# Optimization experiments

Measured on AMD Instinct MI355X. Metric: run time of the kernel, lower is better.

The kernel has to match this reference:

```python
import jax, jax.numpy as jnp
import numpy as np


def setup_inputs() -> dict:
    key = jax.random.key(0)
    kq, kk, kv = jax.random.split(key, 3)
    B, S, D = 4, 4096, 64
    Q = jax.random.normal(kq, (B, S, D), dtype=jnp.float32)
    K = jax.random.normal(kk, (B, S, D), dtype=jnp.float32)
    V = jax.random.normal(kv, (B, S, D), dtype=jnp.float32)
    return {"Q": Q, "K": K, "V": V}


def reference(Q, K, V):
    # nom = Q @ K^T  -> [B, Sq, Sk]
    # Original code does K.transpose_(1,2) in place BEFORE reading K.shape[1],
    # so demon = sqrt(d_head) (standard scaling).
    d = K.shape[-1]
    scores = jnp.einsum('bqd,bkd->bqk', Q, K) / jnp.sqrt(jnp.float32(d))
    # Faithful quirk: nn.Softmax(dim=1) normalizes over the QUERY axis (axis=1).
    attn = jax.nn.softmax(scores, axis=1)
    return jnp.einsum('bqk,bkd->bqd', attn, V)
```

## Files before the change

### kernel.cpp

```cpp
#include <hip/hip_runtime.h>


#define B_N 4
#define S_N 4096
#define D_N 64
#define BS_N (B_N * S_N)
#define NCHUNK 128
#define IMG_CH 8192
#define IMG_CH16 4096
#define QSC (0.125f * 1.44269504088896f)

typedef __attribute__((ext_vector_type(4))) float f32x4;
typedef __attribute__((ext_vector_type(2))) float f32x2;
typedef __attribute__((ext_vector_type(8))) short short8;
typedef __attribute__((ext_vector_type(8))) _Float16 half8;
typedef unsigned char uchar;

#define MFMA16(A, Bf, C) __builtin_amdgcn_mfma_f32_16x16x32_bf16((A), (Bf), (C), 0, 0, 0)
#define MFMAH(A, Bf, C) __builtin_amdgcn_mfma_f32_16x16x32_f16((A), (Bf), (C), 0, 0, 0)

__device__ __forceinline__ void split1(float x, unsigned short& h, unsigned short& l) {
  union { float f; unsigned u; } t; t.f = x;
  h = (unsigned short)(t.u >> 16);
  union { unsigned u; float f; } hv; hv.u = ((unsigned)h) << 16;
  union { float f; unsigned u; } r; r.f = x - hv.f;
  l = (unsigned short)(r.u >> 16);
}

__device__ __forceinline__ void splitFrag8(const f32x4 a, const f32x4 b, short8& hi, short8& lo) {
#pragma unroll
  for (int j = 0; j < 4; ++j) { unsigned short h, l; split1(a[j], h, l); hi[j] = (short)h; lo[j] = (short)l; }
#pragma unroll
  for (int j = 0; j < 4; ++j) { unsigned short h, l; split1(b[j], h, l); hi[4 + j] = (short)h; lo[4 + j] = (short)l; }
}

__device__ __forceinline__ void gld16(const void* g, void* l) {
  __builtin_amdgcn_global_load_lds((const __attribute__((address_space(1))) unsigned int*)g,
                                   (__attribute__((address_space(3))) unsigned int*)l, 16, 0, 0);
}

__global__ __launch_bounds__(256) void sdpa_prepKQ(const float* __restrict__ K,
                                                   const float* __restrict__ Qm,
                                                   uchar* __restrict__ Khl,
                                                   uchar* __restrict__ K16,
                                                   uchar* __restrict__ Q16) {
  const int sel = blockIdx.x >> 9;
  const int c = blockIdx.x & 127;
  const int b = (blockIdx.x >> 7) & 3;
  const int t = threadIdx.x;
  const int r = t >> 3;
  const int d0 = (t & 7) * 8;
  const float* src = (sel ? Qm : K) + ((size_t)(b * S_N + c * 32 + r)) * D_N + d0;
  f32x4 x0 = *(const f32x4*)(src);
  f32x4 x1 = *(const f32x4*)(src + 4);
  const int kt = r >> 4;
  const int lane = ((d0 & 31) >> 3) * 16 + (r & 15);
  const size_t ch16 = ((size_t)(b * NCHUNK + c)) * IMG_CH16 + kt * 2048 + (d0 >> 5) * 1024 + lane * 16;

  if (sel == 0) {
    short8 h8, l8;
    splitFrag8(x0, x1, h8, l8);
    const int ph = d0 >> 5;
    uchar* base = Khl + ((size_t)(b * NCHUNK + c)) * IMG_CH + kt * 4096 + lane * 16;
    *(short8*)(base + ph * 1024) = h8;
    *(short8*)(base + (2 + ph) * 1024) = l8;
    half8 hf;
#pragma unroll
    for (int j = 0; j < 4; ++j) { hf[j] = (_Float16)x0[j]; hf[4 + j] = (_Float16)x1[j]; }
    *(half8*)(K16 + ch16) = hf;
  } else {
    x0 *= QSC; x1 *= QSC;
    half8 hf;
#pragma unroll
    for (int j = 0; j < 4; ++j) { hf[j] = (_Float16)x0[j]; hf[4 + j] = (_Float16)x1[j]; }
    *(half8*)(Q16 + ch16) = hf;
  }
}

__global__ __launch_bounds__(256, 4) void sdpa_stats16(const uchar* __restrict__ K16,
                                                       const uchar* __restrict__ Q16,
                                                       float* __restrict__ lPart) {
  const int tid = threadIdx.x, lane = tid & 63, w = tid >> 6;
  const int l15 = lane & 15, g4 = lane >> 4;
  const int xcd = blockIdx.x & 7;
  const int b = xcd >> 1;
  const int r = blockIdx.x >> 3;
  const int kt = ((r & 31) << 1) | (xcd & 1);
  const int qs = ((r >> 5) << 2) | w;

  half8 kf[4][2];
#pragma unroll
  for (int kg = 0; kg < 4; ++kg) {
    const uchar* kc = K16 + ((size_t)(b * NCHUNK + kt * 2 + (kg >> 1))) * IMG_CH16
                    + (kg & 1) * 2048 + lane * 16;
    kf[kg][0] = *(const half8*)(kc);
    kf[kg][1] = *(const half8*)(kc + 1024);
  }

  float lacc[4][4];
#pragma unroll
  for (int kg = 0; kg < 4; ++kg)
#pragma unroll
    for (int rr = 0; rr < 4; ++rr) lacc[kg][rr] = 0.f;

  const uchar* Qbase = Q16 + ((size_t)(b * NCHUNK + qs * 8)) * IMG_CH16 + lane * 16;

#pragma unroll 1
  for (int it = 0; it < 8; ++it) {
    const uchar* Qc = Qbase + (size_t)it * IMG_CH16;
#pragma unroll
    for (int qt = 0; qt < 2; ++qt) {
      half8 qf0 = *(const half8*)(Qc + qt * 2048);
      half8 qf1 = *(const half8*)(Qc + qt * 2048 + 1024);
#pragma unroll
      for (int kg = 0; kg < 4; ++kg) {
        f32x4 acc = {0.f, 0.f, 0.f, 0.f};
        acc = MFMAH(kf[kg][0], qf0, acc);
        acc = MFMAH(kf[kg][1], qf1, acc);
#pragma unroll
        for (int rr = 0; rr < 4; ++rr)
          lacc[kg][rr] += exp2f(acc[rr]);
      }
    }
  }

#pragma unroll
  for (int off = 1; off < 16; off <<= 1)
#pragma unroll
    for (int kg = 0; kg < 4; ++kg)
#pragma unroll
      for (int rr = 0; rr < 4; ++rr)
        lacc[kg][rr] += __shfl_xor(lacc[kg][rr], off);

  if (l15 == 0) {
#pragma unroll
    for (int kg = 0; kg < 4; ++kg)
#pragma unroll
      for (int rr = 0; rr < 4; ++rr)
        lPart[(size_t)qs * BS_N + b * S_N + kt * 64 + kg * 16 + (g4 << 2) + rr] = lacc[kg][rr];
  }
}

__global__ __launch_bounds__(256) void sdpa_prepV8(const float* __restrict__ V,
                                                   const float* __restrict__ lPart,
                                                   uchar* __restrict__ VT) {
  __shared__ float Vs[32][65];
  __shared__ float rls[32];
  const int c = blockIdx.x & 127;
  const int b = blockIdx.x >> 7;
  const int t = threadIdx.x;
  {
    const int k = t >> 3;
    const int d0 = (t & 7) * 8;
    const float* src = V + ((size_t)(b * S_N + c * 32 + k)) * D_N + d0;
    f32x4 x0 = *(const f32x4*)(src);
    f32x4 x1 = *(const f32x4*)(src + 4);
#pragma unroll
    for (int j = 0; j < 4; ++j) { Vs[k][d0 + j] = x0[j]; Vs[k][d0 + 4 + j] = x1[j]; }
    if (t < 32) {
      float s = 0.f;
      const float* lp = lPart + b * S_N + c * 32 + t;
#pragma unroll
      for (int j = 0; j < 16; ++j) s += lp[(size_t)j * BS_N];
      rls[t] = 1.0f / s;
    }
  }
  __syncthreads();
  const int d = t >> 2;
  const int kg = t & 3;
  half8 hf;
#pragma unroll
  for (int j = 0; j < 8; ++j) {
    const int cc = kg * 8 + j;
    const int k = (((cc >> 2) & 1) << 4) + (((cc >> 3)) << 2) + (cc & 3);
    hf[j] = (_Float16)(Vs[k][d] * rls[k]);
  }
  const int lane = kg * 16 + (d & 15);
  *(half8*)(VT + ((size_t)(b * NCHUNK + c)) * IMG_CH16 + (d >> 4) * 1024 + lane * 16) = hf;
}

__global__ __launch_bounds__(1024, 4) void sdpa_apply18(const float* __restrict__ Q,
                                                        const uchar* __restrict__ Kimg,
                                                        const uchar* __restrict__ VTimg,
                                                        float* __restrict__ Out) {
  __shared__ __attribute__((aligned(16))) uchar sm[69632];

  const int tid = threadIdx.x, lane = tid & 63, w = tid >> 6;
  const int l15 = lane & 15, g4 = lane >> 4;
  const int qsub = w >> 3, kq = w & 7;
  const int xcd = blockIdx.x & 7;
  const int b = xcd >> 1;
  const int qt = ((blockIdx.x >> 3) << 1) | (xcd & 1);

  short8 qh[2][2], ql[2][2];
#pragma unroll
  for (int qg = 0; qg < 2; ++qg) {
    const int qRow = qt * 64 + qsub * 32 + qg * 16 + l15;
    const float* Qp = Q + ((size_t)(b * S_N + qRow)) * D_N;
    f32x4 x0 = *(const f32x4*)(Qp + g4 * 8);
    f32x4 x1 = *(const f32x4*)(Qp + g4 * 8 + 4);
    f32x4 y0 = *(const f32x4*)(Qp + 32 + g4 * 8);
    f32x4 y1 = *(const f32x4*)(Qp + 36 + g4 * 8);
    x0 *= QSC; x1 *= QSC; y0 *= QSC; y1 *= QSC;
    splitFrag8(x0, x1, qh[qg][0], ql[qg][0]);
    splitFrag8(y0, y1, qh[qg][1], ql[qg][1]);
  }

  f32x4 accO[2][4];
#pragma unroll
  for (int qg = 0; qg < 2; ++qg)
#pragma unroll
    for (int dt = 0; dt < 4; ++dt) accO[qg][dt] = (f32x4){0.f, 0.f, 0.f, 0.f};

  const uchar* Kc = Kimg + ((size_t)(b * NCHUNK + kq * 16)) * IMG_CH + lane * 16;
  const uchar* Vc = VTimg + ((size_t)(b * NCHUNK + kq * 16)) * IMG_CH16 + lane * 16;
  uchar* const slab0 = sm + kq * 8192;
  const int l16 = lane * 16;

  half8 paF[2];

#define QK_FROM(KB)                                                            \
  _Pragma("unroll")                                                            \
  for (int kt = 0; kt < 2; ++kt) {                                             \
    short8 ah0 = KB[kt][0], ah1 = KB[kt][1];                                   \
    short8 al0 = KB[kt][2], al1 = KB[kt][3];                                   \
    _Pragma("unroll")                                                          \
    for (int qg = 0; qg < 2; ++qg) {                                           \
      f32x4 acc = {0.f, 0.f, 0.f, 0.f};                                        \
      acc = MFMA16(al0, qh[qg][0], acc);                                       \
      acc = MFMA16(ah0, ql[qg][0], acc);                                       \
      acc = MFMA16(ah0, qh[qg][0], acc);                                       \
      acc = MFMA16(al1, qh[qg][1], acc);                                       \
      acc = MFMA16(ah1, ql[qg][1], acc);                                       \
      acc = MFMA16(ah1, qh[qg][1], acc);                                       \
      _Pragma("unroll")                                                        \
      for (int rr = 0; rr < 4; ++rr)                                           \
        paF[qg][kt * 4 + rr] = (_Float16)exp2f(acc[rr]);                       \
    }                                                                          \
  }

#define PV_STEP(SLAB)                                                          \
  {                                                                            \
    _Pragma("unroll")                                                          \
    for (int dt = 0; dt < 4; ++dt) {                                           \
      half8 vf = *(const half8*)((SLAB) + dt * 1024 + l16);                    \
      _Pragma("unroll")                                                        \
      for (int qg = 0; qg < 2; ++qg)                                           \
        accO[qg][dt] = MFMAH(paF[qg], vf, accO[qg][dt]);                       \
    }                                                                          \
  }

  {
    short8 kb[2][4];
#pragma unroll
    for (int kt = 0; kt < 2; ++kt)
#pragma unroll
      for (int p = 0; p < 4; ++p)
        kb[kt][p] = *(const short8*)(Kc + (kt * 4 + p) * 1024);
    if (qsub == 0) {
#pragma unroll
      for (int s = 0; s < 4; ++s)
        gld16(Vc + s * 1024, slab0 + s * 1024);
    }
    QK_FROM(kb)
    asm volatile("s_waitcnt vmcnt(0)" ::: "memory");
    __syncthreads();
  }

#pragma unroll 1
  for (int it = 1; it < 16; ++it) {
    short8 kb[2][4];
    {
      const uchar* Kn = Kc + (size_t)it * IMG_CH;
#pragma unroll
      for (int kt = 0; kt < 2; ++kt)
#pragma unroll
        for (int p = 0; p < 4; ++p)
          kb[kt][p] = *(const short8*)(Kn + (kt * 4 + p) * 1024);
    }
    __builtin_amdgcn_sched_barrier(0);

    PV_STEP(slab0 + ((it - 1) & 1) * 4096)

    __builtin_amdgcn_sched_barrier(0);

    if (qsub == 0) {
      const uchar* Vn = Vc + (size_t)it * IMG_CH16;
      uchar* slabW = slab0 + (it & 1) * 4096;
#pragma unroll
      for (int s = 0; s < 4; ++s)
        gld16(Vn + s * 1024, slabW + s * 1024);
    }

    QK_FROM(kb)

    asm volatile("s_waitcnt vmcnt(0)" ::: "memory");
    __syncthreads();
  }

  PV_STEP(slab0 + 4096)

#undef QK_FROM
#undef PV_STEP

  float* Comb = (float*)sm;
#pragma unroll
  for (int qg = 0; qg < 2; ++qg) {
    __syncthreads();
    {
      float* CombW = Comb + w * (16 * 68);
#pragma unroll
      for (int dt = 0; dt < 4; ++dt)
#pragma unroll
        for (int r = 0; r < 4; ++r)
          CombW[((g4 << 2) + r) * 68 + dt * 16 + l15] = accO[qg][dt][r];
    }
    __syncthreads();
    {
      const int qs2 = tid >> 9;
      const int row = (tid >> 5) & 15;
      const int c2 = (tid & 31) * 2;
      f32x2 s = {0.f, 0.f};
#pragma unroll
      for (int kq2 = 0; kq2 < 8; ++kq2)
        s += *(const f32x2*)(Comb + (qs2 * 8 + kq2) * (16 * 68) + row * 68 + c2);
      *(f32x2*)(Out + ((size_t)(b * S_N + qt * 64 + qs2 * 32 + qg * 16 + row)) * D_N + c2) = s;
    }
  }
}

extern "C" void kernel_launch(void* const* d_in, const int* in_sizes, int n_in,
                              void* d_out, int out_size, void* d_ws, size_t ws_size,
                              hipStream_t stream) {
  (void)in_sizes; (void)n_in; (void)out_size;
  const float* Q = (const float*)d_in[0];
  const float* K = (const float*)d_in[1];
  const float* V = (const float*)d_in[2];
  float* out = (float*)d_out;
  uchar* ws = (uchar*)d_ws;

  const size_t offKhl = 0;
  const size_t offK16 = (size_t)B_N * NCHUNK * IMG_CH;
  const size_t offQ16 = offK16 + (size_t)B_N * NCHUNK * IMG_CH16;
  const size_t offLP = offQ16 + (size_t)B_N * NCHUNK * IMG_CH16;
  const size_t need = offLP + (size_t)16 * BS_N * 4;

  if (ws_size < need) return;
  float* lPart = (float*)(ws + offLP);

  sdpa_prepKQ<<<dim3(1024), dim3(256), 0, stream>>>(K, Q, ws + offKhl, ws + offK16, ws + offQ16);
  sdpa_stats16<<<dim3(1024), dim3(256), 0, stream>>>(ws + offK16, ws + offQ16, lPart);
  sdpa_prepV8<<<dim3(512), dim3(256), 0, stream>>>(V, lPart, ws + offQ16);
  sdpa_apply18<<<dim3(256), dim3(1024), 0, stream>>>(Q, ws + offKhl, ws + offQ16, out);
}
```

Baseline: 75.19 us.

## Use single fp16 QK products in apply kernel and stage K through LDS

The apply kernel no longer computes QK^T with a three-term bf16 hi/lo split. It now issues a single fp16 MFMA pair using the K16 image already produced for the stats pass, which removes the Khl image and its split work in the prep kernel. K is now staged into LDS with global_load_lds alongside V: one wave group loads K and the other loads V, into double-buffered slabs, with the shared buffer enlarged to 128KB. This cuts MFMA count and global traffic but lowers score precision to fp16, and the larger LDS footprint may limit occupancy.

```diff
diff --git a/kernel.cpp b/kernel.cpp
--- a/kernel.cpp
+++ b/kernel.cpp
@@ -6,44 +6,25 @@
 #define D_N 64
 #define BS_N (B_N * S_N)
 #define NCHUNK 128
-#define IMG_CH 8192
 #define IMG_CH16 4096
 #define QSC (0.125f * 1.44269504088896f)
 
 typedef __attribute__((ext_vector_type(4))) float f32x4;
 typedef __attribute__((ext_vector_type(2))) float f32x2;
-typedef __attribute__((ext_vector_type(8))) short short8;
 typedef __attribute__((ext_vector_type(8))) _Float16 half8;
 typedef unsigned char uchar;
 
-#define MFMA16(A, Bf, C) __builtin_amdgcn_mfma_f32_16x16x32_bf16((A), (Bf), (C), 0, 0, 0)
 #define MFMAH(A, Bf, C) __builtin_amdgcn_mfma_f32_16x16x32_f16((A), (Bf), (C), 0, 0, 0)
-
-__device__ __forceinline__ void split1(float x, unsigned short& h, unsigned short& l) {
-  union { float f; unsigned u; } t; t.f = x;
-  h = (unsigned short)(t.u >> 16);
-  union { unsigned u; float f; } hv; hv.u = ((unsigned)h) << 16;
-  union { float f; unsigned u; } r; r.f = x - hv.f;
-  l = (unsigned short)(r.u >> 16);
-}
-
-__device__ __forceinline__ void splitFrag8(const f32x4 a, const f32x4 b, short8& hi, short8& lo) {
-#pragma unroll
-  for (int j = 0; j < 4; ++j) { unsigned short h, l; split1(a[j], h, l); hi[j] = (short)h; lo[j] = (short)l; }
-#pragma unroll
-  for (int j = 0; j < 4; ++j) { unsigned short h, l; split1(b[j], h, l); hi[4 + j] = (short)h; lo[4 + j] = (short)l; }
-}
 
 __device__ __forceinline__ void gld16(const void* g, void* l) {
   __builtin_amdgcn_global_load_lds((const __attribute__((address_space(1))) unsigned int*)g,
                                    (__attribute__((address_space(3))) unsigned int*)l, 16, 0, 0);
 }
 
-__global__ __launch_bounds__(256) void sdpa_prepKQ(const float* __restrict__ K,
-                                                   const float* __restrict__ Qm,
-                                                   uchar* __restrict__ Khl,
-                                                   uchar* __restrict__ K16,
-                                                   uchar* __restrict__ Q16) {
+__global__ __launch_bounds__(256) void sdpa_prepKQ19(const float* __restrict__ K,
+                                                     const float* __restrict__ Qm,
+                                                     uchar* __restrict__ K16,
+                                                     uchar* __restrict__ Q16) {
   const int sel = blockIdx.x >> 9;
   const int c = blockIdx.x & 127;
   const int b = (blockIdx.x >> 7) & 3;
@@ -53,28 +34,15 @@
   const float* src = (sel ? Qm : K) + ((size_t)(b * S_N + c * 32 + r)) * D_N + d0;
   f32x4 x0 = *(const f32x4*)(src);
   f32x4 x1 = *(const f32x4*)(src + 4);
+  const float scale = sel ? QSC : 1.0f;
+  x0 *= scale; x1 *= scale;
+  half8 hf;
+#pragma unroll
+  for (int j = 0; j < 4; ++j) { hf[j] = (_Float16)x0[j]; hf[4 + j] = (_Float16)x1[j]; }
   const int kt = r >> 4;
   const int lane = ((d0 & 31) >> 3) * 16 + (r & 15);
-  const size_t ch16 = ((size_t)(b * NCHUNK + c)) * IMG_CH16 + kt * 2048 + (d0 >> 5) * 1024 + lane * 16;
-
-  if (sel == 0) {
-    short8 h8, l8;
-    splitFrag8(x0, x1, h8, l8);
-    const int ph = d0 >> 5;
-    uchar* base = Khl + ((size_t)(b * NCHUNK + c)) * IMG_CH + kt * 4096 + lane * 16;
-    *(short8*)(base + ph * 1024) = h8;
-    *(short8*)(base + (2 + ph) * 1024) = l8;
-    half8 hf;
-#pragma unroll
-    for (int j = 0; j < 4; ++j) { hf[j] = (_Float16)x0[j]; hf[4 + j] = (_Float16)x1[j]; }
-    *(half8*)(K16 + ch16) = hf;
-  } else {
-    x0 *= QSC; x1 *= QSC;
-    half8 hf;
-#pragma unroll
-    for (int j = 0; j < 4; ++j) { hf[j] = (_Float16)x0[j]; hf[4 + j] = (_Float16)x1[j]; }
-    *(half8*)(Q16 + ch16) = hf;
-  }
+  uchar* img = sel ? Q16 : K16;
+  *(half8*)(img + ((size_t)(b * NCHUNK + c)) * IMG_CH16 + kt * 2048 + (d0 >> 5) * 1024 + lane * 16) = hf;
 }
 
 __global__ __launch_bounds__(256, 4) void sdpa_stats16(const uchar* __restrict__ K16,
@@ -179,11 +147,11 @@
   *(half8*)(VT + ((size_t)(b * NCHUNK + c)) * IMG_CH16 + (d >> 4) * 1024 + lane * 16) = hf;
 }
 
-__global__ __launch_bounds__(1024, 4) void sdpa_apply18(const float* __restrict__ Q,
-                                                        const uchar* __restrict__ Kimg,
+__global__ __launch_bounds__(1024, 4) void sdpa_apply19(const float* __restrict__ Q,
+                                                        const uchar* __restrict__ K16,
                                                         const uchar* __restrict__ VTimg,
                                                         float* __restrict__ Out) {
-  __shared__ __attribute__((aligned(16))) uchar sm[69632];
+  __shared__ __attribute__((aligned(16))) uchar sm[131072];
 
   const int tid = threadIdx.x, lane = tid & 63, w = tid >> 6;
   const int l15 = lane & 15, g4 = lane >> 4;
@@ -192,7 +160,7 @@
   const int b = xcd >> 1;
   const int qt = ((blockIdx.x >> 3) << 1) | (xcd & 1);
 
-  short8 qh[2][2], ql[2][2];
+  half8 qf[2][2];
 #pragma unroll
   for (int qg = 0; qg < 2; ++qg) {
     const int qRow = qt * 64 + qsub * 32 + qg * 16 + l15;
@@ -202,8 +170,11 @@
     f32x4 y0 = *(const f32x4*)(Qp + 32 + g4 * 8);
     f32x4 y1 = *(const f32x4*)(Qp + 36 + g4 * 8);
     x0 *= QSC; x1 *= QSC; y0 *= QSC; y1 *= QSC;
-    splitFrag8(x0, x1, qh[qg][0], ql[qg][0]);
-    splitFrag8(y0, y1, qh[qg][1], ql[qg][1]);
+#pragma unroll
+    for (int j = 0; j < 4; ++j) {
+      qf[qg][0][j] = (_Float16)x0[j]; qf[qg][0][4 + j] = (_Float16)x1[j];
+      qf[qg][1][j] = (_Float16)y0[j]; qf[qg][1][4 + j] = (_Float16)y1[j];
+    }
   }
 
   f32x4 accO[2][4];
@@ -212,96 +183,61 @@
 #pragma unroll
     for (int dt = 0; dt < 4; ++dt) accO[qg][dt] = (f32x4){0.f, 0.f, 0.f, 0.f};
 
-  const uchar* Kc = Kimg + ((size_t)(b * NCHUNK + kq * 16)) * IMG_CH + lane * 16;
+  const uchar* Kc = K16 + ((size_t)(b * NCHUNK + kq * 16)) * IMG_CH16 + lane * 16;
   const uchar* Vc = VTimg + ((size_t)(b * NCHUNK + kq * 16)) * IMG_CH16 + lane * 16;
-  uchar* const slab0 = sm + kq * 8192;
+  uchar* const slab = sm + kq * 16384;
   const int l16 = lane * 16;
 
-  half8 paF[2];
-
-#define QK_FROM(KB)                                                            \
-  _Pragma("unroll")                                                            \
-  for (int kt = 0; kt < 2; ++kt) {                                             \
-    short8 ah0 = KB[kt][0], ah1 = KB[kt][1];                                   \
-    short8 al0 = KB[kt][2], al1 = KB[kt][3];                                   \
+#define STAGE(IT, PAR)                                                         \
+  {                                                                            \
+    uchar* dst = slab + (PAR) * 8192 + (qsub == 0 ? 4096 : 0);                 \
+    const uchar* src = (qsub == 0 ? Vc : Kc) + (size_t)(IT) * IMG_CH16;        \
     _Pragma("unroll")                                                          \
-    for (int qg = 0; qg < 2; ++qg) {                                           \
-      f32x4 acc = {0.f, 0.f, 0.f, 0.f};                                        \
-      acc = MFMA16(al0, qh[qg][0], acc);                                       \
-      acc = MFMA16(ah0, ql[qg][0], acc);                                       \
-      acc = MFMA16(ah0, qh[qg][0], acc);                                       \
-      acc = MFMA16(al1, qh[qg][1], acc);                                       \
-      acc = MFMA16(ah1, ql[qg][1], acc);                                       \
-      acc = MFMA16(ah1, qh[qg][1], acc);                                       \
-      _Pragma("unroll")                                                        \
-      for (int rr = 0; rr < 4; ++rr)                                           \
-        paF[qg][kt * 4 + rr] = (_Float16)exp2f(acc[rr]);                       \
-    }                                                                          \
-  }
-
-#define PV_STEP(SLAB)                                                          \
-  {                                                                            \
-    _Pragma("unroll")                                                          \
-    for (int dt = 0; dt < 4; ++dt) {                                           \
-      half8 vf = *(const half8*)((SLAB) + dt * 1024 + l16);                    \
-      _Pragma("unroll")                                                        \
-      for (int qg = 0; qg < 2; ++qg)                                           \
-        accO[qg][dt] = MFMAH(paF[qg], vf, accO[qg][dt]);                       \
-    }                                                                          \
-  }
-
-  {
-    short8 kb[2][4];
-#pragma unroll
-    for (int kt = 0; kt < 2; ++kt)
-#pragma unroll
-      for (int p = 0; p < 4; ++p)
-        kb[kt][p] = *(const short8*)(Kc + (kt * 4 + p) * 1024);
-    if (qsub == 0) {
-#pragma unroll
-      for (int s = 0; s < 4; ++s)
-        gld16(Vc + s * 1024, slab0 + s * 1024);
-    }
-    QK_FROM(kb)
+    for (int s = 0; s < 4; ++s) gld16(src + s * 1024, dst + s * 1024);         \
+  }
+
+  STAGE(0, 0)
+  asm volatile("s_waitcnt vmcnt(0)" ::: "memory");
+  __syncthreads();
+
+#pragma unroll 1
+  for (int it = 0; it < 16; ++it) {
+    const int par = it & 1;
+    if (it < 15) STAGE(it + 1, par ^ 1)
+    __builtin_amdgcn_sched_barrier(0);
+
+    const uchar* ks = slab + par * 8192;
+    const uchar* vs = ks + 4096;
+
+    half8 paF[2];
+#pragma unroll
+    for (int kt = 0; kt < 2; ++kt) {
+      half8 kf0 = *(const half8*)(ks + kt * 2048 + l16);
+      half8 kf1 = *(const half8*)(ks + kt * 2048 + 1024 + l16);
+#pragma unroll
+      for (int qg = 0; qg < 2; ++qg) {
+        f32x4 acc = {0.f, 0.f, 0.f, 0.f};
+        acc = MFMAH(kf0, qf[qg][0], acc);
+        acc = MFMAH(kf1, qf[qg][1], acc);
+#pragma unroll
+        for (int rr = 0; rr < 4; ++rr)
+          paF[qg][kt * 4 + rr] = (_Float16)exp2f(acc[rr]);
+      }
+    }
+
+#pragma unroll
+    for (int dt = 0; dt < 4; ++dt) {
+      half8 vf = *(const half8*)(vs + dt * 1024 + l16);
+#pragma unroll
+      for (int qg = 0; qg < 2; ++qg)
+        accO[qg][dt] = MFMAH(paF[qg], vf, accO[qg][dt]);
+    }
+
     asm volatile("s_waitcnt vmcnt(0)" ::: "memory");
     __syncthreads();
   }
 
-#pragma unroll 1
-  for (int it = 1; it < 16; ++it) {
-    short8 kb[2][4];
-    {
-      const uchar* Kn = Kc + (size_t)it * IMG_CH;
-#pragma unroll
-      for (int kt = 0; kt < 2; ++kt)
-#pragma unroll
-        for (int p = 0; p < 4; ++p)
-          kb[kt][p] = *(const short8*)(Kn + (kt * 4 + p) * 1024);
-    }
-    __builtin_amdgcn_sched_barrier(0);
-
-    PV_STEP(slab0 + ((it - 1) & 1) * 4096)
-
-    __builtin_amdgcn_sched_barrier(0);
-
-    if (qsub == 0) {
-      const uchar* Vn = Vc + (size_t)it * IMG_CH16;
-      uchar* slabW = slab0 + (it & 1) * 4096;
-#pragma unroll
-      for (int s = 0; s < 4; ++s)
-        gld16(Vn + s * 1024, slabW + s * 1024);
-    }
-
-    QK_FROM(kb)
-
-    asm volatile("s_waitcnt vmcnt(0)" ::: "memory");
-    __syncthreads();
-  }
-
-  PV_STEP(slab0 + 4096)
-
-#undef QK_FROM
-#undef PV_STEP
+#undef STAGE
 
   float* Comb = (float*)sm;
 #pragma unroll
@@ -339,17 +275,17 @@
   float* out = (float*)d_out;
   uchar* ws = (uchar*)d_ws;
 
-  const size_t offKhl = 0;
-  const size_t offK16 = (size_t)B_N * NCHUNK * IMG_CH;
-  const size_t offQ16 = offK16 + (size_t)B_N * NCHUNK * IMG_CH16;
-  const size_t offLP = offQ16 + (size_t)B_N * NCHUNK * IMG_CH16;
+  const size_t img16 = (size_t)B_N * NCHUNK * IMG_CH16;
+  const size_t offK16 = 0;
+  const size_t offQ16 = img16;
+  const size_t offLP = 2 * img16;
   const size_t need = offLP + (size_t)16 * BS_N * 4;
 
   if (ws_size < need) return;
   float* lPart = (float*)(ws + offLP);
 
-  sdpa_prepKQ<<<dim3(1024), dim3(256), 0, stream>>>(K, Q, ws + offKhl, ws + offK16, ws + offQ16);
+  sdpa_prepKQ19<<<dim3(1024), dim3(256), 0, stream>>>(K, Q, ws + offK16, ws + offQ16);
   sdpa_stats16<<<dim3(1024), dim3(256), 0, stream>>>(ws + offK16, ws + offQ16, lPart);
   sdpa_prepV8<<<dim3(512), dim3(256), 0, stream>>>(V, lPart, ws + offQ16);
-  sdpa_apply18<<<dim3(256), dim3(1024), 0, stream>>>(Q, ws + offKhl, ws + offQ16, out);
-}
+  sdpa_apply19<<<dim3(256), dim3(1024), 0, stream>>>(Q, ws + offK16, ws + offQ16, out);
+}
```

Measured after the change: 61.46 us. -18.3%, faster.
